# Kernel tuning notes

Measured on AMD Instinct MI355X. Metric: run time of the kernel, lower is better.

Reference implementation:

```python
import jax, jax.numpy as jnp
import numpy as np

HIDDEN = 1024
HEADS = 16
HEAD_DIM = HIDDEN // HEADS
SCALE = float(np.sqrt(HEAD_DIM))
B, S = 4, 2048


def setup_inputs() -> dict:
    key = jax.random.key(0)
    ks = jax.random.split(key, 10)
    inp = {
        "query": jax.random.normal(ks[0], (B, S, HIDDEN), dtype=jnp.float32),
        "mask": jax.random.randint(ks[1], (B, S), 0, 2).astype(jnp.bool_),
        "Wq": jax.random.normal(ks[2], (HIDDEN, HIDDEN), dtype=jnp.float32) * 0.02,
        "bq": jax.random.normal(ks[3], (HIDDEN,), dtype=jnp.float32) * 0.02,
        "Wk": jax.random.normal(ks[4], (HIDDEN, HIDDEN), dtype=jnp.float32) * 0.02,
        "bk": jax.random.normal(ks[5], (HIDDEN,), dtype=jnp.float32) * 0.02,
        "Wv": jax.random.normal(ks[6], (HIDDEN, HIDDEN), dtype=jnp.float32) * 0.02,
        "bv": jax.random.normal(ks[7], (HIDDEN,), dtype=jnp.float32) * 0.02,
        "Wo": jax.random.normal(ks[8], (HIDDEN, HIDDEN), dtype=jnp.float32) * 0.02,
        "bo": jax.random.normal(ks[9], (HIDDEN,), dtype=jnp.float32) * 0.02,
    }
    return inp


def reference(query, mask, Wq, bq, Wk, bk, Wv, bv, Wo, bo):
    b, s, _ = query.shape
    # QKV projections (torch Linear: x @ W.T + b)
    q = query @ Wq.T + bq
    k = query @ Wk.T + bk
    v = query @ Wv.T + bv
    # [b, h, s, d]
    q = q.reshape(b, s, HEADS, HEAD_DIM).transpose(0, 2, 1, 3)
    k = k.reshape(b, s, HEADS, HEAD_DIM).transpose(0, 2, 1, 3)
    v = v.reshape(b, s, HEADS, HEAD_DIM).transpose(0, 2, 1, 3)
    # energy[b,h,i,j] = q_i . k_j / scale
    energy = jnp.einsum("bhid,bhjd->bhij", q, k) / SCALE
    m = mask.astype(energy.dtype)
    energy = energy * m[:, None, :, None] * m[:, None, None, :]
    # NOTE: softmax over the QUERY axis (dim=2), not the key axis
    attention = jax.nn.softmax(energy, axis=2)
    x = jnp.einsum("bhij,bhjd->bhid", attention, v)
    x = x.transpose(0, 2, 1, 3).reshape(b, s, HIDDEN)
    out = x @ Wo.T + bo
    return jnp.squeeze(out)
```

## Files before the change

### kernel.cpp

```cpp
#include <hip/hip_runtime.h>

#define SQ   2048
#define HIDN 1024
#define NB   4
#define NH   16
#define HD   64

typedef __attribute__((ext_vector_type(8))) short short8;
typedef __attribute__((ext_vector_type(4))) short short4v;
typedef __attribute__((ext_vector_type(4))) float f32x4;

__device__ __forceinline__ short f2bf(float f) {
  union { float f; unsigned u; } x; x.f = f;
  unsigned r = (x.u + 0x7fffu + ((x.u >> 16) & 1u)) >> 16;
  return (short)r;
}

__device__ __forceinline__ unsigned cvtpk_bf16(float lo, float hi) {
  unsigned u;
  asm("v_cvt_pk_bf16_f32 %0, %1, %2" : "=v"(u) : "v"(lo), "v"(hi));
  return u;
}

__device__ __forceinline__ float exp2_raw(float x) {
  float r;
  asm("v_exp_f32 %0, %1" : "=v"(r) : "v"(x));
  return r;
}

#define MFMA(a, b, c) __builtin_amdgcn_mfma_f32_16x16x32_bf16((a), (b), (c), 0, 0, 0)

__device__ __forceinline__ void gload16(const void* g, void* l) {
  __builtin_amdgcn_global_load_lds(
      (const __attribute__((address_space(1))) unsigned*)g,
      (__attribute__((address_space(3))) unsigned*)l, 16, 0, 0);
}

#define LOG2E 1.44269504f

__global__ __launch_bounds__(256) void k_maskprep(const unsigned* __restrict__ mraw,
                                                  float* __restrict__ m) {
  __shared__ unsigned red[256];
  const int tid = threadIdx.x;
  unsigned w_or = 0;
  for (int i = tid; i < 2048; i += 256) w_or |= mraw[i];
  red[tid] = w_or;
  __syncthreads();
  for (int s = 128; s > 0; s >>= 1) {
    if (tid < s) red[tid] |= red[tid + s];
    __syncthreads();
  }
  const unsigned allw = red[0];
  int mode;
  if ((allw & 0xFFFFFFFEu) == 0) mode = 0;
  else if ((allw & 0xFEFEFEFEu) == 0) mode = 1;
  else mode = 2;
  const unsigned char* mb = (const unsigned char*)mraw;
  const float* mf = (const float*)mraw;
  const int* mi = (const int*)mraw;
  for (int i = tid; i < NB * SQ; i += 256) {
    float v;
    if (mode == 0)      v = mi[i] ? 1.0f : 0.0f;
    else if (mode == 1) v = mb[i] ? 1.0f : 0.0f;
    else                v = (mf[i] != 0.0f) ? 1.0f : 0.0f;
    m[i] = v;
  }
}

__global__ __launch_bounds__(256) void k_cvt(
    const float* __restrict__ query, const float* __restrict__ Wq,
    const float* __restrict__ Wk, const float* __restrict__ Wv,
    short* __restrict__ qbf, short* __restrict__ wbf)
{
  const int yy = blockIdx.y;
  const float* __restrict__ src = (yy == 0) ? query : (yy == 1) ? Wq : (yy == 2) ? Wk : Wv;
  short* __restrict__ dst = (yy == 0) ? qbf : wbf + (yy - 1) * (HIDN * HIDN);
  const int n = (yy == 0) ? (NB * SQ * HIDN) : (HIDN * HIDN);
  const int i = (blockIdx.x * 256 + threadIdx.x) * 4;
  if (i >= n) return;
  const f32x4 v = *(const f32x4*)(src + i);
  short4v s;
#pragma unroll
  for (int e = 0; e < 4; ++e) s[e] = f2bf(v[e]);
  *(short4v*)(dst + i) = s;
}

__global__ __launch_bounds__(256) void k_cvtWo(
    const float* __restrict__ Wo, short* __restrict__ wo)
{
  const int i = (blockIdx.x * 256 + threadIdx.x) * 4;
  if (i >= HIDN * HIDN) return;
  const f32x4 v = *(const f32x4*)(Wo + i);
  short4v s;
#pragma unroll
  for (int e = 0; e < 4; ++e) s[e] = f2bf(v[e]);
  *(short4v*)(wo + i) = s;
}

__global__ __launch_bounds__(256) void k_proj_qkv2(
    const short* __restrict__ qbf, const short* __restrict__ wbf,
    const float* __restrict__ bq, const float* __restrict__ bkb,
    const float* __restrict__ bv, const float* __restrict__ mfl,
    short* __restrict__ qh, short* __restrict__ kh, short* __restrict__ vh)
{
  __shared__ short a_s[2][128 * 64];
  __shared__ short b_s[2][128 * 64];
  const int nt = blockIdx.x, mt = blockIdx.y;
  const int tid = threadIdx.x;
  const int w = tid >> 6, lane = tid & 63;
  const int wr = w >> 1, wc = w & 1;
  const int lg = lane >> 4, lr = lane & 15;

  const int z = nt >> 3;
  const float* __restrict__ bias = (z == 0) ? bq : (z == 1) ? bkb : bv;

  int srow[4], scs[4], sbase[4];
#pragma unroll
  for (int p = 0; p < 4; ++p) {
    const int id = p * 256 + tid;
    const int r = id >> 3, c = id & 7;
    srow[p] = r;
    scs[p] = c ^ (r & 7);
    sbase[p] = (p * 256 + w * 64) * 8;
  }

  f32x4 acc[4][4] = {};

#pragma unroll
  for (int p = 0; p < 4; ++p) {
    gload16(qbf + (size_t)(mt * 128 + srow[p]) * HIDN + scs[p] * 8, a_s[0] + sbase[p]);
    gload16(wbf + (size_t)(nt * 128 + srow[p]) * HIDN + scs[p] * 8, b_s[0] + sbase[p]);
  }
  __syncthreads();

  int cur = 0;
  for (int k0 = 0; k0 < HIDN; k0 += 64) {
    if (k0 + 64 < HIDN) {
      const int kn = k0 + 64;
#pragma unroll
      for (int p = 0; p < 4; ++p) {
        gload16(qbf + (size_t)(mt * 128 + srow[p]) * HIDN + kn + scs[p] * 8,
                a_s[cur ^ 1] + sbase[p]);
        gload16(wbf + (size_t)(nt * 128 + srow[p]) * HIDN + kn + scs[p] * 8,
                b_s[cur ^ 1] + sbase[p]);
      }
    }
#pragma unroll
    for (int kk = 0; kk < 2; ++kk) {
      short8 af[4], bfv[4];
#pragma unroll
      for (int mi = 0; mi < 4; ++mi) {
        const int r = wr * 64 + mi * 16 + lr;
        const int phys = (kk * 4 + lg) ^ (r & 7);
        af[mi] = *(const short8*)((const char*)a_s[cur] + r * 128 + phys * 16);
      }
#pragma unroll
      for (int ni = 0; ni < 4; ++ni) {
        const int r = wc * 64 + ni * 16 + lr;
        const int phys = (kk * 4 + lg) ^ (r & 7);
        bfv[ni] = *(const short8*)((const char*)b_s[cur] + r * 128 + phys * 16);
      }
#pragma unroll
      for (int mi = 0; mi < 4; ++mi)
#pragma unroll
        for (int ni = 0; ni < 4; ++ni)
          acc[mi][ni] = MFMA(af[mi], bfv[ni], acc[mi][ni]);
    }
    __syncthreads();
    cur ^= 1;
  }

#pragma unroll
  for (int mi = 0; mi < 4; ++mi)
#pragma unroll
    for (int ni = 0; ni < 4; ++ni)
#pragma unroll
      for (int r = 0; r < 4; ++r) {
        const int row = mt * 128 + wr * 64 + mi * 16 + lg * 4 + r;
        const int colz = (nt & 7) * 128 + wc * 64 + ni * 16 + lr;
        const float v = acc[mi][ni][r] + bias[colz];
        const int bi = row >> 11, s = row & (SQ - 1);
        const int h = colz >> 6, d = colz & (HD - 1);
        const int idx = ((bi * NH + h) * SQ + s) * HD + d;
        if (z == 0) {
          qh[idx] = f2bf(v * (0.125f * LOG2E) * mfl[row]);
        } else if (z == 1) {
          kh[idx] = f2bf(v * mfl[row]);
        } else {
          vh[idx] = f2bf(v);
        }
      }
}

__global__ __launch_bounds__(256) void k_sumexp_m(
    const short* __restrict__ qh, const short* __restrict__ kh,
    float* __restrict__ rcpL)
{
  __shared__ short q_s[2][64][72];
  const int bh = blockIdx.y;
  const int jt = blockIdx.x;
  const int tid = threadIdx.x, w = tid >> 6, lane = tid & 63;
  const int lg = lane >> 4, lr = lane & 15;

  const int base = bh * SQ * HD;
  const int jbase = jt * 256 + w * 64;

  short8 bk[4][2];
#pragma unroll
  for (int jf = 0; jf < 4; ++jf) {
    const int j = jbase + jf * 16 + lr;
    bk[jf][0] = *(const short8*)(kh + base + j * HD + lg * 8);
    bk[jf][1] = *(const short8*)(kh + base + j * HD + 32 + lg * 8);
  }

  const int srow = tid >> 3, scc = (tid & 7) * 8;
  {
    const short8 s0 = *(const short8*)(qh + base + srow * HD + scc);
    const short8 s1 = *(const short8*)(qh + base + (32 + srow) * HD + scc);
    *(short8*)&q_s[0][srow][scc] = s0;
    *(short8*)&q_s[0][32 + srow][scc] = s1;
  }
  __syncthreads();

  f32x4 Lacc[4] = {};
  for (int t = 0; t < 32; ++t) {
    const int cur = t & 1;
    short8 n0, n1;
    if (t < 31) {
      const int ibn = (t + 1) * 64;
      n0 = *(const short8*)(qh + base + (ibn + srow) * HD + scc);
      n1 = *(const short8*)(qh + base + (ibn + 32 + srow) * HD + scc);
    }
#pragma unroll
    for (int s = 0; s < 4; ++s) {
      const short8 a0 = *(const short8*)&q_s[cur][s * 16 + lr][lg * 8];
      const short8 a1 = *(const short8*)&q_s[cur][s * 16 + lr][32 + lg * 8];
#pragma unroll
      for (int jf = 0; jf < 4; ++jf) {
        f32x4 e = {};
        e = MFMA(a0, bk[jf][0], e);
        e = MFMA(a1, bk[jf][1], e);
#pragma unroll
        for (int r = 0; r < 4; ++r)
          Lacc[jf][r] += exp2_raw(e[r]);
      }
    }
    if (t < 31) {
      __syncthreads();
      *(short8*)&q_s[cur ^ 1][srow][scc] = n0;
      *(short8*)&q_s[cur ^ 1][32 + srow][scc] = n1;
      __syncthreads();
    }
  }

#pragma unroll
  for (int jf = 0; jf < 4; ++jf) {
    float L = Lacc[jf][0] + Lacc[jf][1] + Lacc[jf][2] + Lacc[jf][3];
    L += __shfl_xor(L, 16, 64);
    L += __shfl_xor(L, 32, 64);
    if (lg == 0) rcpL[bh * SQ + jbase + jf * 16 + lr] = 1.0f / L;
  }
}

__global__ __launch_bounds__(256) void k_vtrans(
    const short* __restrict__ vh, const float* __restrict__ rcpL,
    short* __restrict__ vT)
{
  __shared__ short t[64][72];
  const int bh = blockIdx.y;
  const int s0 = blockIdx.x * 64;
  const int tid = threadIdx.x;
  const int base = bh * SQ * HD;
#pragma unroll
  for (int p = 0; p < 2; ++p) {
    const int id = p * 256 + tid;
    const int r = id >> 3, c = id & 7;
    const short8 v = *(const short8*)(vh + base + (s0 + r) * HD + c * 8);
    const float sc = rcpL[bh * SQ + s0 + r];
    float f[8];
#pragma unroll
    for (int e = 0; e < 8; ++e) {
      union { unsigned u; float x; } cv;
      cv.u = ((unsigned)(unsigned short)v[e]) << 16;
      f[e] = cv.x * sc;
    }
    union { unsigned u[4]; short8 s8; } o;
#pragma unroll
    for (int e = 0; e < 4; ++e) o.u[e] = cvtpk_bf16(f[2 * e], f[2 * e + 1]);
    *(short8*)&t[r][c * 8] = o.s8;
  }
  __syncthreads();
  const int d = tid >> 2, sc4 = (tid & 3) * 16;
  short val[16];
#pragma unroll
  for (int k = 0; k < 16; ++k) val[k] = t[sc4 + k][d];
  *(short8*)(vT + base + d * SQ + s0 + sc4) = *(const short8*)&val[0];
  *(short8*)(vT + base + d * SQ + s0 + sc4 + 8) = *(const short8*)&val[8];
}

__global__ __launch_bounds__(256) void k_attnv(
    const short* __restrict__ qh, const short* __restrict__ kh,
    const short* __restrict__ vT,
    short* __restrict__ xo)
{
  __shared__ short k_s[64 * 64];
  __shared__ short v_s[64 * 64];
  __shared__ __attribute__((aligned(16))) short p_s[4][4][16][40];
  const int bh = blockIdx.y, b = bh >> 4, h = bh & (NH - 1);
  const int it = blockIdx.x;
  const int tid = threadIdx.x, w = tid >> 6, lane = tid & 63;
  const int lg = lane >> 4, lr = lane & 15;

  const int base = bh * SQ * HD;
  const int i0 = it * 256 + w * 64;

  short8 aq[4][2];
#pragma unroll
  for (int fi = 0; fi < 4; ++fi) {
    aq[fi][0] = *(const short8*)(qh + base + (i0 + fi * 16 + lr) * HD + lg * 8);
    aq[fi][1] = *(const short8*)(qh + base + (i0 + fi * 16 + lr) * HD + 32 + lg * 8);
  }

  int strow[2], stphys[2], stbase[2];
#pragma unroll
  for (int p = 0; p < 2; ++p) {
    const int id = p * 256 + tid;
    const int r = id >> 3, c = id & 7;
    strow[p] = r;
    stphys[p] = c ^ (r & 7);
    stbase[p] = (p * 256 + w * 64) * 8;
  }

  f32x4 accx[4][4] = {};
  for (int jb = 0; jb < SQ; jb += 64) {
#pragma unroll
    for (int p = 0; p < 2; ++p) {
      gload16(kh + base + (size_t)(jb + strow[p]) * HD + stphys[p] * 8,
              k_s + stbase[p]);
      gload16(vT + base + (size_t)strow[p] * SQ + jb + stphys[p] * 8,
              v_s + stbase[p]);
    }
    __syncthreads();

#pragma unroll
    for (int sub = 0; sub < 2; ++sub) {
      short8 bk[2][2];
#pragma unroll
      for (int jj = 0; jj < 2; ++jj) {
        const int rr = sub * 32 + jj * 16 + lr;
        const int ph0 = lg ^ (rr & 7);
        const int ph1 = (4 + lg) ^ (rr & 7);
        bk[jj][0] = *(const short8*)(k_s + rr * 64 + ph0 * 8);
        bk[jj][1] = *(const short8*)(k_s + rr * 64 + ph1 * 8);
      }
      short8 bv[4];
#pragma unroll
      for (int nd = 0; nd < 4; ++nd) {
        const int rv = nd * 16 + lr;
        const int ph = (sub * 4 + lg) ^ (rv & 7);
        bv[nd] = *(const short8*)(v_s + rv * 64 + ph * 8);
      }

#pragma unroll
      for (int fi = 0; fi < 4; ++fi) {
        f32x4 e0 = {}, e1 = {};
        e0 = MFMA(bk[0][0], aq[fi][0], e0);
        e0 = MFMA(bk[0][1], aq[fi][1], e0);
        e1 = MFMA(bk[1][0], aq[fi][0], e1);
        e1 = MFMA(bk[1][1], aq[fi][1], e1);
        const unsigned u00 = cvtpk_bf16(exp2_raw(e0[0]), exp2_raw(e0[1]));
        const unsigned u01 = cvtpk_bf16(exp2_raw(e0[2]), exp2_raw(e0[3]));
        const unsigned u10 = cvtpk_bf16(exp2_raw(e1[0]), exp2_raw(e1[1]));
        const unsigned u11 = cvtpk_bf16(exp2_raw(e1[2]), exp2_raw(e1[3]));
        uint2 w0; w0.x = u00; w0.y = u01;
        uint2 w1; w1.x = u10; w1.y = u11;
        *(uint2*)&p_s[w][fi][lr][lg * 4] = w0;
        *(uint2*)&p_s[w][fi][lr][16 + lg * 4] = w1;
      }
#pragma unroll
      for (int fi = 0; fi < 4; ++fi) {
        const short8 pa = *(const short8*)&p_s[w][fi][lr][lg * 8];
#pragma unroll
        for (int nd = 0; nd < 4; ++nd)
          accx[fi][nd] = MFMA(pa, bv[nd], accx[fi][nd]);
      }
    }
    __syncthreads();
  }

#pragma unroll
  for (int fi = 0; fi < 4; ++fi)
#pragma unroll
    for (int nd = 0; nd < 4; ++nd)
#pragma unroll
      for (int r = 0; r < 4; ++r) {
        const int i = i0 + fi * 16 + lg * 4 + r, d = nd * 16 + lr;
        xo[(b * SQ + i) * HIDN + h * HD + d] = f2bf(accx[fi][nd][r]);
      }
}

__global__ __launch_bounds__(256) void k_proj_out2(
    const short* __restrict__ xb, const short* __restrict__ wo,
    const float* __restrict__ bo, float* __restrict__ out)
{
  __shared__ short a_s[2][128 * 64];
  __shared__ short b_s[2][128 * 64];
  const int nt = blockIdx.x, mt = blockIdx.y;
  const int tid = threadIdx.x;
  const int w = tid >> 6, lane = tid & 63;
  const int wr = w >> 1, wc = w & 1;
  const int lg = lane >> 4, lr = lane & 15;

  int srow[4], scs[4], sbase[4];
#pragma unroll
  for (int p = 0; p < 4; ++p) {
    const int id = p * 256 + tid;
    const int r = id >> 3, c = id & 7;
    srow[p] = r;
    scs[p] = c ^ (r & 7);
    sbase[p] = (p * 256 + w * 64) * 8;
  }

  f32x4 acc[4][4] = {};

#pragma unroll
  for (int p = 0; p < 4; ++p) {
    gload16(xb + (size_t)(mt * 128 + srow[p]) * HIDN + scs[p] * 8, a_s[0] + sbase[p]);
    gload16(wo + (size_t)(nt * 128 + srow[p]) * HIDN + scs[p] * 8, b_s[0] + sbase[p]);
  }
  __syncthreads();

  int cur = 0;
  for (int k0 = 0; k0 < HIDN; k0 += 64) {
    if (k0 + 64 < HIDN) {
      const int kn = k0 + 64;
#pragma unroll
      for (int p = 0; p < 4; ++p) {
        gload16(xb + (size_t)(mt * 128 + srow[p]) * HIDN + kn + scs[p] * 8,
                a_s[cur ^ 1] + sbase[p]);
        gload16(wo + (size_t)(nt * 128 + srow[p]) * HIDN + kn + scs[p] * 8,
                b_s[cur ^ 1] + sbase[p]);
      }
    }
#pragma unroll
    for (int kk = 0; kk < 2; ++kk) {
      short8 af[4], bfv[4];
#pragma unroll
      for (int mi = 0; mi < 4; ++mi) {
        const int r = wr * 64 + mi * 16 + lr;
        const int phys = (kk * 4 + lg) ^ (r & 7);
        af[mi] = *(const short8*)((const char*)a_s[cur] + r * 128 + phys * 16);
      }
#pragma unroll
      for (int ni = 0; ni < 4; ++ni) {
        const int r = wc * 64 + ni * 16 + lr;
        const int phys = (kk * 4 + lg) ^ (r & 7);
        bfv[ni] = *(const short8*)((const char*)b_s[cur] + r * 128 + phys * 16);
      }
#pragma unroll
      for (int mi = 0; mi < 4; ++mi)
#pragma unroll
        for (int ni = 0; ni < 4; ++ni)
          acc[mi][ni] = MFMA(af[mi], bfv[ni], acc[mi][ni]);
    }
    __syncthreads();
    cur ^= 1;
  }

#pragma unroll
  for (int mi = 0; mi < 4; ++mi)
#pragma unroll
    for (int ni = 0; ni < 4; ++ni)
#pragma unroll
      for (int r = 0; r < 4; ++r) {
        const int row = mt * 128 + wr * 64 + mi * 16 + lg * 4 + r;
        const int col = nt * 128 + wc * 64 + ni * 16 + lr;
        out[row * HIDN + col] = acc[mi][ni][r] + bo[col];
      }
}

extern "C" void kernel_launch(void* const* d_in, const int* in_sizes, int n_in,
                              void* d_out, int out_size, void* d_ws, size_t ws_size,
                              hipStream_t stream) {
  const float* query = (const float*)d_in[0];
  const unsigned* mraw = (const unsigned*)d_in[1];
  const float* Wq = (const float*)d_in[2];
  const float* bq = (const float*)d_in[3];
  const float* Wk = (const float*)d_in[4];
  const float* bk = (const float*)d_in[5];
  const float* Wv = (const float*)d_in[6];
  const float* bv = (const float*)d_in[7];
  const float* Wo = (const float*)d_in[8];
  const float* bo = (const float*)d_in[9];

  short* qh  = (short*)d_ws;
  short* kh  = qh + (NB * NH * SQ * HD);
  short* vT  = kh + (NB * NH * SQ * HD);
  short* xb  = vT + (NB * NH * SQ * HD);
  float* rcpL = (float*)(xb + (NB * SQ * HIDN));
  float* mfl = rcpL + (NB * NH * SQ);

  short* vh = xb;

  short* qbf = (short*)d_out;
  short* wbf = qbf + (NB * SQ * HIDN);
  short* wo  = qh;

  k_maskprep<<<dim3(1), dim3(256), 0, stream>>>(mraw, mfl);
  k_cvt<<<dim3((NB * SQ * HIDN) / 1024, 4), dim3(256), 0, stream>>>(
      query, Wq, Wk, Wv, qbf, wbf);
  k_proj_qkv2<<<dim3(24, 64), dim3(256), 0, stream>>>(
      qbf, wbf, bq, bk, bv, mfl, qh, kh, vh);
  k_sumexp_m<<<dim3(SQ / 256, NB * NH), dim3(256), 0, stream>>>(qh, kh, rcpL);
  k_vtrans<<<dim3(SQ / 64, NB * NH), dim3(256), 0, stream>>>(vh, rcpL, vT);
  k_attnv<<<dim3(SQ / 256, NB * NH), dim3(256), 0, stream>>>(qh, kh, vT, xb);
  k_cvtWo<<<dim3((HIDN * HIDN) / 1024), dim3(256), 0, stream>>>(Wo, wo);
  k_proj_out2<<<dim3(HIDN / 128, (NB * SQ) / 128), dim3(256), 0, stream>>>(
      xb, wo, bo, (float*)d_out);
}
```

Before: 282.7 us.

## Enlarge QKV projection tile to 256x256 with 512-thread blocks, single-buffered

The QKV projection GEMM moves from 128x128 tiles with 256 threads and double-buffered LDS to 256x256 tiles with 512 threads (8 waves in a 2x4 layout), each wave computing 128x64. The larger tile raises operand reuse per byte loaded and halves the grid. Double buffering is dropped, so global-to-LDS loads no longer overlap MFMA work and each k-step now waits on two barriers. Per-thread accumulator count doubles, which raises register pressure and may lower occupancy; the grid shrinks to 384 blocks, which may underfill the GPU.

After: 306.0 us. +8.2%, slower.

```diff
diff --git a/kernel.cpp b/kernel.cpp
--- a/kernel.cpp
+++ b/kernel.cpp
@@ -97,87 +97,76 @@
   *(short4v*)(wo + i) = s;
 }
 
-__global__ __launch_bounds__(256) void k_proj_qkv2(
+__global__ __launch_bounds__(512) void k_proj_qkv3(
     const short* __restrict__ qbf, const short* __restrict__ wbf,
     const float* __restrict__ bq, const float* __restrict__ bkb,
     const float* __restrict__ bv, const float* __restrict__ mfl,
     short* __restrict__ qh, short* __restrict__ kh, short* __restrict__ vh)
 {
-  __shared__ short a_s[2][128 * 64];
-  __shared__ short b_s[2][128 * 64];
+  __shared__ short a_s[256 * 64];
+  __shared__ short b_s[256 * 64];
   const int nt = blockIdx.x, mt = blockIdx.y;
   const int tid = threadIdx.x;
   const int w = tid >> 6, lane = tid & 63;
-  const int wr = w >> 1, wc = w & 1;
+  const int wr = w >> 2, wc = w & 3;
   const int lg = lane >> 4, lr = lane & 15;
 
-  const int z = nt >> 3;
+  const int z = nt >> 2;
   const float* __restrict__ bias = (z == 0) ? bq : (z == 1) ? bkb : bv;
 
   int srow[4], scs[4], sbase[4];
 #pragma unroll
   for (int p = 0; p < 4; ++p) {
-    const int id = p * 256 + tid;
+    const int id = p * 512 + tid;
     const int r = id >> 3, c = id & 7;
     srow[p] = r;
     scs[p] = c ^ (r & 7);
-    sbase[p] = (p * 256 + w * 64) * 8;
-  }
-
-  f32x4 acc[4][4] = {};
-
-#pragma unroll
-  for (int p = 0; p < 4; ++p) {
-    gload16(qbf + (size_t)(mt * 128 + srow[p]) * HIDN + scs[p] * 8, a_s[0] + sbase[p]);
-    gload16(wbf + (size_t)(nt * 128 + srow[p]) * HIDN + scs[p] * 8, b_s[0] + sbase[p]);
-  }
-  __syncthreads();
-
-  int cur = 0;
+    sbase[p] = (p * 512 + w * 64) * 8;
+  }
+
+  f32x4 acc[8][4] = {};
+
   for (int k0 = 0; k0 < HIDN; k0 += 64) {
-    if (k0 + 64 < HIDN) {
-      const int kn = k0 + 64;
-#pragma unroll
-      for (int p = 0; p < 4; ++p) {
-        gload16(qbf + (size_t)(mt * 128 + srow[p]) * HIDN + kn + scs[p] * 8,
-                a_s[cur ^ 1] + sbase[p]);
-        gload16(wbf + (size_t)(nt * 128 + srow[p]) * HIDN + kn + scs[p] * 8,
-                b_s[cur ^ 1] + sbase[p]);
-      }
-    }
+#pragma unroll
+    for (int p = 0; p < 4; ++p) {
+      gload16(qbf + (size_t)(mt * 256 + srow[p]) * HIDN + k0 + scs[p] * 8,
+              a_s + sbase[p]);
+      gload16(wbf + (size_t)(nt * 256 + srow[p]) * HIDN + k0 + scs[p] * 8,
+              b_s + sbase[p]);
+    }
+    __syncthreads();
 #pragma unroll
     for (int kk = 0; kk < 2; ++kk) {
-      short8 af[4], bfv[4];
-#pragma unroll
-      for (int mi = 0; mi < 4; ++mi) {
-        const int r = wr * 64 + mi * 16 + lr;
+      short8 af[8], bfv[4];
+#pragma unroll
+      for (int mi = 0; mi < 8; ++mi) {
+        const int r = wr * 128 + mi * 16 + lr;
         const int phys = (kk * 4 + lg) ^ (r & 7);
-        af[mi] = *(const short8*)((const char*)a_s[cur] + r * 128 + phys * 16);
+        af[mi] = *(const short8*)((const char*)a_s + r * 128 + phys * 16);
       }
 #pragma unroll
       for (int ni = 0; ni < 4; ++ni) {
         const int r = wc * 64 + ni * 16 + lr;
         const int phys = (kk * 4 + lg) ^ (r & 7);
-        bfv[ni] = *(const short8*)((const char*)b_s[cur] + r * 128 + phys * 16);
-      }
-#pragma unroll
-      for (int mi = 0; mi < 4; ++mi)
+        bfv[ni] = *(const short8*)((const char*)b_s + r * 128 + phys * 16);
+      }
+#pragma unroll
+      for (int mi = 0; mi < 8; ++mi)
 #pragma unroll
         for (int ni = 0; ni < 4; ++ni)
           acc[mi][ni] = MFMA(af[mi], bfv[ni], acc[mi][ni]);
     }
     __syncthreads();
-    cur ^= 1;
-  }
-
-#pragma unroll
-  for (int mi = 0; mi < 4; ++mi)
+  }
+
+#pragma unroll
+  for (int mi = 0; mi < 8; ++mi)
 #pragma unroll
     for (int ni = 0; ni < 4; ++ni)
 #pragma unroll
       for (int r = 0; r < 4; ++r) {
-        const int row = mt * 128 + wr * 64 + mi * 16 + lg * 4 + r;
-        const int colz = (nt & 7) * 128 + wc * 64 + ni * 16 + lr;
+        const int row = mt * 256 + wr * 128 + mi * 16 + lg * 4 + r;
+        const int colz = (nt & 3) * 256 + wc * 64 + ni * 16 + lr;
         const float v = acc[mi][ni][r] + bias[colz];
         const int bi = row >> 11, s = row & (SQ - 1);
         const int h = colz >> 6, d = colz & (HD - 1);
@@ -509,7 +498,7 @@
   k_maskprep<<<dim3(1), dim3(256), 0, stream>>>(mraw, mfl);
   k_cvt<<<dim3((NB * SQ * HIDN) / 1024, 4), dim3(256), 0, stream>>>(
       query, Wq, Wk, Wv, qbf, wbf);
-  k_proj_qkv2<<<dim3(24, 64), dim3(256), 0, stream>>>(
+  k_proj_qkv3<<<dim3(12, 32), dim3(512), 0, stream>>>(
       qbf, wbf, bq, bk, bv, mfl, qh, kh, vh);
   k_sumexp_m<<<dim3(SQ / 256, NB * NH), dim3(256), 0, stream>>>(qh, kh, rcpL);
   k_vtrans<<<dim3(SQ / 64, NB * NH), dim3(256), 0, stream>>>(vh, rcpL, vT);
```
